# Kernel tuning notes

Measured on AMD Instinct MI355X. Metric: run time of the kernel, lower is better.

Reference implementation:

```python
import jax, jax.numpy as jnp
import numpy as np

DPH = 64          # dim_per_head
HALF = DPH // 2   # rope half dim
NH = 8            # num heads
SCALE = jnp.sqrt(jnp.float32(DPH))


def setup_inputs() -> dict:
    key = jax.random.key(0)
    ks = jax.random.split(key, 6)
    b, H, W, d = 2, 48, 48, 512
    qk_bound = 6.0 / np.sqrt(d + DPH)
    x = jax.random.normal(ks[0], (b, H, W, d), dtype=jnp.float32)
    wq = jax.random.uniform(ks[1], (d, DPH, NH), jnp.float32, -qk_bound, qk_bound)
    wk = jax.random.uniform(ks[2], (d, DPH, NH), jnp.float32, -qk_bound, qk_bound)
    wv = jax.random.uniform(ks[3], (d, DPH, NH), jnp.float32, -qk_bound, qk_bound)
    wo = jax.random.uniform(ks[4], (d, DPH, NH), jnp.float32, -qk_bound, qk_bound)
    angles = jax.random.normal(ks[5], (2, HALF), dtype=jnp.float32)  # base_freq=1.0
    return {"x": x, "wq": wq, "wk": wk, "wv": wv, "wo": wo, "angles": angles}


def _rope_angles(H, W, angles):
    # positions: meshgrid(indexing='ij') of arange(H), arange(W) -> [H, W, 2]
    ii, jj = jnp.meshgrid(jnp.arange(H, dtype=angles.dtype),
                          jnp.arange(W, dtype=angles.dtype), indexing="ij")
    pos = jnp.stack([ii, jj], axis=-1)              # [H, W, 2]
    return jnp.einsum("ijp,pc->ijc", pos, angles)   # [H, W, HALF]


def _apply_rope(t, cos, sin):
    # t: [b, h, H, W, dv]; interleaved pairs (d c) with c=2
    tr = t.reshape(*t.shape[:-1], HALF, 2)
    t0, t1 = tr[..., 0], tr[..., 1]
    rot = jnp.stack([t0 * cos - t1 * sin, t0 * sin + t1 * cos], axis=-1)
    return rot.reshape(t.shape)


def reference(x, wq, wk, wv, wo, angles):
    b, H, W, d = x.shape
    # QKV projections: [b,H,W,d] x [d,dv,h] -> [b,h,H,W,dv]
    q = jnp.einsum("bijd,dvh->bhijv", x, wq)
    k = jnp.einsum("bijd,dvh->bhijv", x, wk)
    v = jnp.einsum("bijd,dvh->bhijv", x, wv)
    ang = _rope_angles(H, W, angles)
    cos, sin = jnp.cos(ang), jnp.sin(ang)           # [H, W, HALF]
    q = _apply_rope(q, cos, sin)
    k = _apply_rope(k, cos, sin)
    # flatten spatial dims -> sequence
    n = H * W
    qf = q.reshape(b, NH, n, DPH)
    kf = k.reshape(b, NH, n, DPH)
    vf = v.reshape(b, NH, n, DPH)
    scores = jnp.einsum("bhqd,bhkd->bhqk", qf, kf) / SCALE
    attn = jax.nn.softmax(scores, axis=-1)
    out = jnp.einsum("bhqk,bhkd->bhqd", attn, vf).reshape(b, NH, H, W, DPH)
    # out projection: [b,h,H,W,dv] x [d,dv,h] -> [b,H,W,d]
    return jnp.einsum("bhijv,dvh->bijd", out, wo)
```

## Files before the change

### kernel.cpp

```cpp
#include <hip/hip_runtime.h>
#include <hip/hip_bf16.h>
#include <math.h>

#define BB   2
#define WW   48
#define DD   512
#define DPH  64
#define NHH  8
#define NSEQ 2304
#define NPOS (BB*NSEQ)
#define NXE  (NPOS*DD)
#define WSZ  (DD*DD)

typedef __attribute__((ext_vector_type(8))) short short8v;
typedef __attribute__((ext_vector_type(4))) float f32x4;

__device__ __forceinline__ ushort f2bf(float f) {
    union { __hip_bfloat16 h; ushort u; } cv;
    cv.h = __float2bfloat16(f);
    return cv.u;
}
__device__ __forceinline__ float bf2f(ushort u) {
    return __uint_as_float(((uint)u) << 16);
}

__global__ __launch_bounds__(256) void k_prep(
    const float* __restrict__ x,  const float* __restrict__ wq,
    const float* __restrict__ wk, const float* __restrict__ wv,
    const float* __restrict__ wo,
    ushort* __restrict__ xh, ushort* __restrict__ xl,
    ushort* __restrict__ Bqh, ushort* __restrict__ Bql,
    ushort* __restrict__ Bkh, ushort* __restrict__ Bkl,
    ushort* __restrict__ Bvh, ushort* __restrict__ Bvl,
    ushort* __restrict__ Boh, ushort* __restrict__ Bol)
{
    int idx = blockIdx.x*256 + threadIdx.x;
    float s;
    ushort *ph, *pl; int o;
    if (idx < NXE) {
        s = x[idx]; ph = xh; pl = xl; o = idx;
    } else {
        int t = idx - NXE;
        int sel = t >> 18;
        o = t & (WSZ-1);
        int c = o >> 9, k = o & 511;
        if (sel == 0)      { s = wq[k*512 + c] * 0.125f; ph = Bqh; pl = Bql; }
        else if (sel == 1) { s = wk[k*512 + c];          ph = Bkh; pl = Bkl; }
        else if (sel == 2) { s = wv[k*512 + c];          ph = Bvh; pl = Bvl; }
        else               { s = wo[c*512 + ((k&63)<<3) + (k>>6)]; ph = Boh; pl = Bol; }
    }
    ushort hi = f2bf(s);
    ph[o] = hi;
    pl[o] = f2bf(s - bf2f(hi));
}

#define LPITCH 80
__global__ __launch_bounds__(256) void k_gemm_qkv(
    const ushort* __restrict__ xhp, const ushort* __restrict__ xlp,
    const ushort* __restrict__ Bqh, const ushort* __restrict__ Bql,
    const ushort* __restrict__ Bkh, const ushort* __restrict__ Bkl,
    const ushort* __restrict__ Bvh, const ushort* __restrict__ Bvl,
    const float* __restrict__ ang,
    ushort* __restrict__ qa, ushort* __restrict__ ka, ushort* __restrict__ vT)
{
    __shared__ char xsh[64*LPITCH], xsl[64*LPITCH];
    __shared__ char wsh[256*LPITCH], wsl[256*LPITCH];
    const int tid = threadIdx.x;
    const int w = tid>>6, l = tid&63, g = l>>4, lr = l&15;
    const int mid = blockIdx.x / 144;
    const int rmb = blockIdx.x - mid*144;
    const int rowblk = rmb >> 1, colblk = rmb & 1;
    const int row0 = rowblk*64, col0 = colblk*256;
    const ushort* Bh; const ushort* Bl;
    if (mid==0)      { Bh = Bqh; Bl = Bql; }
    else if (mid==1) { Bh = Bkh; Bl = Bkl; }
    else             { Bh = Bvh; Bl = Bvl; }

    f32x4 acc[4][4];
#pragma unroll
    for (int mt=0;mt<4;++mt)
#pragma unroll
        for (int nt=0;nt<4;++nt) acc[mt][nt] = (f32x4){0.f,0.f,0.f,0.f};

#pragma unroll 1
    for (int kc = 0; kc < 16; ++kc) {
        const int k0 = kc*32;
        __syncthreads();
#pragma unroll
        for (int u = 0; u < 2; ++u) {
            int i2 = tid + 256*u;
            int tile = i2 >> 8, t2 = i2 & 255;
            int sr = t2 >> 2, sg = t2 & 3;
            const ushort* src = (tile ? xlp : xhp) + (size_t)(row0+sr)*512 + k0 + sg*8;
            char* dst = (tile ? xsl : xsh) + sr*LPITCH + sg*16;
            *reinterpret_cast<uint4*>(dst) = *reinterpret_cast<const uint4*>(src);
        }
#pragma unroll
        for (int u = 0; u < 8; ++u) {
            int i2 = tid + 256*u;
            int tile = i2 >> 10, t2 = i2 & 1023;
            int c = t2 >> 2, sg = t2 & 3;
            const ushort* src = (tile ? Bl : Bh) + (size_t)(col0+c)*512 + k0 + sg*8;
            char* dst = (tile ? wsl : wsh) + c*LPITCH + sg*16;
            *reinterpret_cast<uint4*>(dst) = *reinterpret_cast<const uint4*>(src);
        }
        __syncthreads();
        short8v ah[4], al[4], bh_[4], bl_[4];
#pragma unroll
        for (int mt = 0; mt < 4; ++mt) {
            ah[mt] = *reinterpret_cast<const short8v*>(xsh + (mt*16+lr)*LPITCH + g*16);
            al[mt] = *reinterpret_cast<const short8v*>(xsl + (mt*16+lr)*LPITCH + g*16);
        }
#pragma unroll
        for (int nt = 0; nt < 4; ++nt) {
            bh_[nt] = *reinterpret_cast<const short8v*>(wsh + (w*64+nt*16+lr)*LPITCH + g*16);
            bl_[nt] = *reinterpret_cast<const short8v*>(wsl + (w*64+nt*16+lr)*LPITCH + g*16);
        }
#pragma unroll
        for (int mt = 0; mt < 4; ++mt)
#pragma unroll
            for (int nt = 0; nt < 4; ++nt) {
                acc[mt][nt] = __builtin_amdgcn_mfma_f32_16x16x32_bf16(ah[mt], bh_[nt], acc[mt][nt], 0, 0, 0);
                acc[mt][nt] = __builtin_amdgcn_mfma_f32_16x16x32_bf16(ah[mt], bl_[nt], acc[mt][nt], 0, 0, 0);
                acc[mt][nt] = __builtin_amdgcn_mfma_f32_16x16x32_bf16(al[mt], bh_[nt], acc[mt][nt], 0, 0, 0);
            }
    }

    const int b = row0 / NSEQ;
    const int rem0 = row0 - b*NSEQ;
    if (mid < 2) {
        ushort* dst = (mid==0) ? qa : ka;
        const int sgn = (lr >= 8);
#pragma unroll
        for (int nt = 0; nt < 4; ++nt) {
            int cbase = col0 + w*64 + nt*16;
            int pc = cbase >> 4;
            float a_i = ang[pc], a_j = ang[32 + pc];
            int c = cbase + lr;
            int h = c & 7, v = c >> 3;
            ushort* colbase = dst + ((size_t)(b*NHH + h)*NSEQ)*DPH + v;
#pragma unroll
            for (int mt = 0; mt < 4; ++mt)
#pragma unroll
                for (int r = 0; r < 4; ++r) {
                    int rowrem = rem0 + mt*16 + 4*g + r;
                    int i = rowrem / WW, j = rowrem - (rowrem/WW)*WW;
                    float th = (float)i*a_i + (float)j*a_j;
                    float sn, cn; __sincosf(th, &sn, &cn);
                    float own = acc[mt][nt][r];
                    float oth = __shfl_xor(own, 8);
                    float rot = sgn ? (oth*sn + own*cn) : (own*cn - oth*sn);
                    colbase[(size_t)rowrem*DPH] = f2bf(rot);
                }
        }
    } else {
#pragma unroll
        for (int nt = 0; nt < 4; ++nt) {
            int c = col0 + w*64 + nt*16 + lr;
            int h = c & 7, v = c >> 3;
            ushort* colbase = vT + ((size_t)((b*NHH + h)*DPH + v))*NSEQ + rem0;
#pragma unroll
            for (int mt = 0; mt < 4; ++mt)
#pragma unroll
                for (int r = 0; r < 4; ++r)
                    colbase[mt*16 + 4*g + r] = f2bf(acc[mt][nt][r]);
        }
    }
}

__global__ __launch_bounds__(256) void k_gemm_o(
    const ushort* __restrict__ Oa, const ushort* __restrict__ Boh,
    const ushort* __restrict__ Bol, float* __restrict__ out)
{
    __shared__ char xs[64*LPITCH];
    __shared__ char wsh[256*LPITCH], wsl[256*LPITCH];
    const int tid = threadIdx.x;
    const int w = tid>>6, l = tid&63, g = l>>4, lr = l&15;
    const int row0 = (blockIdx.x >> 1)*64;
    const int col0 = (blockIdx.x & 1)*256;

    f32x4 acc[4][4];
#pragma unroll
    for (int mt=0;mt<4;++mt)
#pragma unroll
        for (int nt=0;nt<4;++nt) acc[mt][nt] = (f32x4){0.f,0.f,0.f,0.f};

#pragma unroll 1
    for (int kc = 0; kc < 16; ++kc) {
        const int k0 = kc*32;
        __syncthreads();
        {
            int sr = tid >> 2, sg = tid & 3;
            *reinterpret_cast<uint4*>(xs + sr*LPITCH + sg*16) =
                *reinterpret_cast<const uint4*>(Oa + (size_t)(row0+sr)*512 + k0 + sg*8);
        }
#pragma unroll
        for (int u = 0; u < 8; ++u) {
            int i2 = tid + 256*u;
            int tile = i2 >> 10, t2 = i2 & 1023;
            int c = t2 >> 2, sg = t2 & 3;
            const ushort* src = (tile ? Bol : Boh) + (size_t)(col0+c)*512 + k0 + sg*8;
            char* dst = (tile ? wsl : wsh) + c*LPITCH + sg*16;
            *reinterpret_cast<uint4*>(dst) = *reinterpret_cast<const uint4*>(src);
        }
        __syncthreads();
        short8v a[4], bh_[4], bl_[4];
#pragma unroll
        for (int mt = 0; mt < 4; ++mt)
            a[mt] = *reinterpret_cast<const short8v*>(xs + (mt*16+lr)*LPITCH + g*16);
#pragma unroll
        for (int nt = 0; nt < 4; ++nt) {
            bh_[nt] = *reinterpret_cast<const short8v*>(wsh + (w*64+nt*16+lr)*LPITCH + g*16);
            bl_[nt] = *reinterpret_cast<const short8v*>(wsl + (w*64+nt*16+lr)*LPITCH + g*16);
        }
#pragma unroll
        for (int mt = 0; mt < 4; ++mt)
#pragma unroll
            for (int nt = 0; nt < 4; ++nt) {
                acc[mt][nt] = __builtin_amdgcn_mfma_f32_16x16x32_bf16(a[mt], bh_[nt], acc[mt][nt], 0, 0, 0);
                acc[mt][nt] = __builtin_amdgcn_mfma_f32_16x16x32_bf16(a[mt], bl_[nt], acc[mt][nt], 0, 0, 0);
            }
    }

#pragma unroll
    for (int mt=0;mt<4;++mt)
#pragma unroll
        for (int r=0;r<4;++r) {
            float* rowp = out + (size_t)(row0 + mt*16 + 4*g + r)*DD + col0 + w*64;
#pragma unroll
            for (int nt=0;nt<4;++nt)
                rowp[nt*16 + lr] = acc[mt][nt][r];
        }
}

#define CK 64
#define NCHUNK (NSEQ/CK)
#define KP 72
__global__ __launch_bounds__(256) void k_attn_mfma(
    const ushort* __restrict__ qb, const ushort* __restrict__ kb,
    const ushort* __restrict__ vb, ushort* __restrict__ Oa)
{
    __shared__ ushort ksm[CK][KP];
    __shared__ ushort vsm[CK][KP];
    __shared__ ushort psm[4][16][KP];
    const int tid = threadIdx.x;
    const int w = tid >> 6, l = tid & 63;
    const int g = l >> 4, lr = l & 15;
    const int bh   = blockIdx.x / (NSEQ/64);
    const int qc   = blockIdx.x - bh*(NSEQ/64);
    const int row0 = qc * 64;
    const ushort* kbase = kb + (size_t)bh*NSEQ*DPH;
    const ushort* vbase = vb + (size_t)bh*DPH*NSEQ;

    const ushort* qptr = qb + ((size_t)bh*NSEQ + row0 + 16*w + lr)*DPH + g*8;
    const short8v qA0 = *reinterpret_cast<const short8v*>(qptr);
    const short8v qA1 = *reinterpret_cast<const short8v*>(qptr + 32);

    float mrow[4], lrow[4];
    f32x4 o[4];
#pragma unroll
    for (int r = 0; r < 4; ++r) { mrow[r] = -INFINITY; lrow[r] = 0.f; }
#pragma unroll
    for (int vt = 0; vt < 4; ++vt) o[vt] = (f32x4){0.f,0.f,0.f,0.f};

    for (int t = 0; t < NCHUNK; ++t) {
        __syncthreads();
#pragma unroll
        for (int i = 0; i < 2; ++i) {
            int tau = tid + 256*i;
            int row = tau >> 3, cg = tau & 7;
            *reinterpret_cast<uint4*>(&ksm[row][cg*8]) =
                *reinterpret_cast<const uint4*>(kbase + ((size_t)(t*CK + row))*DPH + cg*8);
            *reinterpret_cast<uint4*>(&vsm[row][cg*8]) =
                *reinterpret_cast<const uint4*>(vbase + (size_t)row*NSEQ + t*CK + cg*8);
        }
        __syncthreads();

        f32x4 s[4];
#pragma unroll
        for (int tile = 0; tile < 4; ++tile) {
            short8v k0 = *reinterpret_cast<const short8v*>(&ksm[tile*16 + lr][g*8]);
            short8v k1 = *reinterpret_cast<const short8v*>(&ksm[tile*16 + lr][32 + g*8]);
            f32x4 a2 = (f32x4){0.f,0.f,0.f,0.f};
            a2 = __builtin_amdgcn_mfma_f32_16x16x32_bf16(qA0, k0, a2, 0, 0, 0);
            a2 = __builtin_amdgcn_mfma_f32_16x16x32_bf16(qA1, k1, a2, 0, 0, 0);
            s[tile] = a2;
        }

        float f_r[4];
#pragma unroll
        for (int r = 0; r < 4; ++r) {
            float cm = fmaxf(fmaxf(s[0][r], s[1][r]), fmaxf(s[2][r], s[3][r]));
#pragma unroll
            for (int msk = 8; msk >= 1; msk >>= 1)
                cm = fmaxf(cm, __shfl_xor(cm, msk));
            float mn = fmaxf(mrow[r], cm);
            f_r[r] = __expf(mrow[r] - mn);
            mrow[r] = mn;
            float rs = 0.f;
#pragma unroll
            for (int tile = 0; tile < 4; ++tile) {
                float p = __expf(s[tile][r] - mn);
                s[tile][r] = p;
                rs += p;
            }
#pragma unroll
            for (int msk = 8; msk >= 1; msk >>= 1)
                rs += __shfl_xor(rs, msk);
            lrow[r] = lrow[r]*f_r[r] + rs;
        }

#pragma unroll
        for (int tile = 0; tile < 4; ++tile)
#pragma unroll
            for (int r = 0; r < 4; ++r)
                psm[w][4*g + r][lr + 16*tile] = f2bf(s[tile][r]);

#pragma unroll
        for (int vt = 0; vt < 4; ++vt)
#pragma unroll
            for (int r = 0; r < 4; ++r)
                o[vt][r] *= f_r[r];

#pragma unroll
        for (int half = 0; half < 2; ++half) {
            short8v pA = *reinterpret_cast<const short8v*>(&psm[w][lr][32*half + g*8]);
#pragma unroll
            for (int vt = 0; vt < 4; ++vt) {
                short8v vf = *reinterpret_cast<const short8v*>(&vsm[vt*16 + lr][32*half + g*8]);
                o[vt] = __builtin_amdgcn_mfma_f32_16x16x32_bf16(pA, vf, o[vt], 0, 0, 0);
            }
        }
    }

    float inv[4];
#pragma unroll
    for (int r = 0; r < 4; ++r) inv[r] = 1.f / lrow[r];
    const int b_ = bh >> 3, h_ = bh & 7;
#pragma unroll
    for (int vt = 0; vt < 4; ++vt)
#pragma unroll
        for (int r = 0; r < 4; ++r)
            Oa[((size_t)(b_*NSEQ + row0 + 16*w + 4*g + r))*DD + h_*64 + vt*16 + lr]
                = f2bf(o[vt][r]*inv[r]);
}

extern "C" void kernel_launch(void* const* d_in, const int* in_sizes, int n_in,
                              void* d_out, int out_size, void* d_ws, size_t ws_size,
                              hipStream_t stream) {
    const float* x   = (const float*)d_in[0];
    const float* wq  = (const float*)d_in[1];
    const float* wk  = (const float*)d_in[2];
    const float* wv  = (const float*)d_in[3];
    const float* wo  = (const float*)d_in[4];
    const float* ang = (const float*)d_in[5];
    float* out = (float*)d_out;

    ushort* xh  = (ushort*)d_ws;
    ushort* xl  = xh + NXE;
    ushort* Bqh = xl + NXE;
    ushort* Bql = Bqh + WSZ;
    ushort* Bkh = Bql + WSZ;
    ushort* Bkl = Bkh + WSZ;
    ushort* Bvh = Bkl + WSZ;
    ushort* Bvl = Bvh + WSZ;
    ushort* Boh = Bvl + WSZ;
    ushort* Bol = Boh + WSZ;
    ushort* qa  = Bol + WSZ;
    ushort* ka  = qa + NXE;
    ushort* vT  = ka + NXE;
    ushort* Oa  = xh;

    k_prep<<<(NXE + 4*WSZ)/256, 256, 0, stream>>>(x, wq, wk, wv, wo,
        xh, xl, Bqh, Bql, Bkh, Bkl, Bvh, Bvl, Boh, Bol);
    k_gemm_qkv<<<432, 256, 0, stream>>>(xh, xl, Bqh, Bql, Bkh, Bkl, Bvh, Bvl,
        ang, qa, ka, vT);
    k_attn_mfma<<<BB*NHH*(NSEQ/CK), 256, 0, stream>>>(qa, ka, vT, Oa);
    k_gemm_o<<<144, 256, 0, stream>>>(Oa, Boh, Bol, out);
}
```

Measured before the change: 237.7 us.

## Split attention KV range in two and merge partials in a combine kernel

The attention kernel now splits the key sequence into two halves, doubling the block count. Each block writes unnormalized partial outputs plus its running max and sum, and a new combine kernel merges the two halves into the final head-interleaved layout. The probability tile in shared memory is also XOR-swizzled to reduce bank conflicts. This aims to fill the GPU better and reduce the tail of the attention grid, at the cost of an extra launch and extra global traffic for the partials.

```diff
diff --git a/kernel.cpp b/kernel.cpp
--- a/kernel.cpp
+++ b/kernel.cpp
@@ -11,6 +11,7 @@
 #define NPOS (BB*NSEQ)
 #define NXE  (NPOS*DD)
 #define WSZ  (DD*DD)
+#define NROWS (BB*NHH*NSEQ)
 
 typedef __attribute__((ext_vector_type(8))) short short8v;
 typedef __attribute__((ext_vector_type(4))) float f32x4;
@@ -234,20 +235,22 @@
 }
 
 #define CK 64
-#define NCHUNK (NSEQ/CK)
 #define KP 72
 __global__ __launch_bounds__(256) void k_attn_mfma(
     const ushort* __restrict__ qb, const ushort* __restrict__ kb,
-    const ushort* __restrict__ vb, ushort* __restrict__ Oa)
+    const ushort* __restrict__ vb, ushort* __restrict__ Op,
+    float2* __restrict__ mlp)
 {
     __shared__ ushort ksm[CK][KP];
     __shared__ ushort vsm[CK][KP];
-    __shared__ ushort psm[4][16][KP];
+    __shared__ char psmb[4][2304];
     const int tid = threadIdx.x;
     const int w = tid >> 6, l = tid & 63;
     const int g = l >> 4, lr = l & 15;
-    const int bh   = blockIdx.x / (NSEQ/64);
-    const int qc   = blockIdx.x - bh*(NSEQ/64);
+    const int sp  = blockIdx.x / 576;
+    const int rest = blockIdx.x - sp*576;
+    const int bh = rest / 36;
+    const int qc = rest - bh*36;
     const int row0 = qc * 64;
     const ushort* kbase = kb + (size_t)bh*NSEQ*DPH;
     const ushort* vbase = vb + (size_t)bh*DPH*NSEQ;
@@ -263,7 +266,7 @@
 #pragma unroll
     for (int vt = 0; vt < 4; ++vt) o[vt] = (f32x4){0.f,0.f,0.f,0.f};
 
-    for (int t = 0; t < NCHUNK; ++t) {
+    for (int t = sp*18; t < sp*18 + 18; ++t) {
         __syncthreads();
 #pragma unroll
         for (int i = 0; i < 2; ++i) {
@@ -276,7 +279,7 @@
         }
         __syncthreads();
 
-        f32x4 s[4];
+        f32x4 sc[4];
 #pragma unroll
         for (int tile = 0; tile < 4; ++tile) {
             short8v k0 = *reinterpret_cast<const short8v*>(&ksm[tile*16 + lr][g*8]);
@@ -284,13 +287,13 @@
             f32x4 a2 = (f32x4){0.f,0.f,0.f,0.f};
             a2 = __builtin_amdgcn_mfma_f32_16x16x32_bf16(qA0, k0, a2, 0, 0, 0);
             a2 = __builtin_amdgcn_mfma_f32_16x16x32_bf16(qA1, k1, a2, 0, 0, 0);
-            s[tile] = a2;
+            sc[tile] = a2;
         }
 
         float f_r[4];
 #pragma unroll
         for (int r = 0; r < 4; ++r) {
-            float cm = fmaxf(fmaxf(s[0][r], s[1][r]), fmaxf(s[2][r], s[3][r]));
+            float cm = fmaxf(fmaxf(sc[0][r], sc[1][r]), fmaxf(sc[2][r], sc[3][r]));
 #pragma unroll
             for (int msk = 8; msk >= 1; msk >>= 1)
                 cm = fmaxf(cm, __shfl_xor(cm, msk));
@@ -300,8 +303,8 @@
             float rs = 0.f;
 #pragma unroll
             for (int tile = 0; tile < 4; ++tile) {
-                float p = __expf(s[tile][r] - mn);
-                s[tile][r] = p;
+                float p = __expf(sc[tile][r] - mn);
+                sc[tile][r] = p;
                 rs += p;
             }
 #pragma unroll
@@ -313,8 +316,10 @@
 #pragma unroll
         for (int tile = 0; tile < 4; ++tile)
 #pragma unroll
-            for (int r = 0; r < 4; ++r)
-                psm[w][4*g + r][lr + 16*tile] = f2bf(s[tile][r]);
+            for (int r = 0; r < 4; ++r) {
+                int bo = (((4*g + r)*144) + (lr + 16*tile)*2) ^ (g << 5);
+                *reinterpret_cast<ushort*>(&psmb[w][bo]) = f2bf(sc[tile][r]);
+            }
 
 #pragma unroll
         for (int vt = 0; vt < 4; ++vt)
@@ -324,7 +329,8 @@
 
 #pragma unroll
         for (int half = 0; half < 2; ++half) {
-            short8v pA = *reinterpret_cast<const short8v*>(&psm[w][lr][32*half + g*8]);
+            int bo = (lr*144 + 64*half + 16*g) ^ (((lr >> 2) & 3) << 5);
+            short8v pA = *reinterpret_cast<const short8v*>(&psmb[w][bo]);
 #pragma unroll
             for (int vt = 0; vt < 4; ++vt) {
                 short8v vf = *reinterpret_cast<const short8v*>(&vsm[vt*16 + lr][32*half + g*8]);
@@ -333,16 +339,44 @@
         }
     }
 
-    float inv[4];
-#pragma unroll
-    for (int r = 0; r < 4; ++r) inv[r] = 1.f / lrow[r];
-    const int b_ = bh >> 3, h_ = bh & 7;
+    ushort* obase = Op + ((size_t)sp*NROWS + (size_t)bh*NSEQ + row0 + 16*w)*64;
 #pragma unroll
     for (int vt = 0; vt < 4; ++vt)
 #pragma unroll
         for (int r = 0; r < 4; ++r)
-            Oa[((size_t)(b_*NSEQ + row0 + 16*w + 4*g + r))*DD + h_*64 + vt*16 + lr]
-                = f2bf(o[vt][r]*inv[r]);
+            obase[(4*g + r)*64 + vt*16 + lr] = f2bf(o[vt][r]);
+    if (lr == 0) {
+#pragma unroll
+        for (int r = 0; r < 4; ++r)
+            mlp[sp*NROWS + bh*NSEQ + row0 + 16*w + 4*g + r] = make_float2(mrow[r], lrow[r]);
+    }
+}
+
+__global__ __launch_bounds__(256) void k_combine(
+    const ushort* __restrict__ Op, const float2* __restrict__ mlp,
+    ushort* __restrict__ Oa)
+{
+    const int tid = threadIdx.x;
+    const int row = blockIdx.x*32 + (tid >> 3);
+    const int c8 = (tid & 7)*8;
+    float2 a = mlp[row], b = mlp[NROWS + row];
+    float M = fmaxf(a.x, b.x);
+    float w0 = __expf(a.x - M), w1 = __expf(b.x - M);
+    float inv = 1.f / (a.y*w0 + b.y*w1);
+    const ushort* p0 = Op + (size_t)row*64 + c8;
+    const ushort* p1 = p0 + (size_t)NROWS*64;
+    uint4 u0 = *reinterpret_cast<const uint4*>(p0);
+    uint4 u1 = *reinterpret_cast<const uint4*>(p1);
+    const ushort* s0 = reinterpret_cast<const ushort*>(&u0);
+    const ushort* s1 = reinterpret_cast<const ushort*>(&u1);
+    ushort res[8];
+#pragma unroll
+    for (int i = 0; i < 8; ++i)
+        res[i] = f2bf((bf2f(s0[i])*w0 + bf2f(s1[i])*w1) * inv);
+    int bh = row / NSEQ, n = row - bh*NSEQ;
+    int b_ = bh >> 3, h_ = bh & 7;
+    ushort* dst = Oa + ((size_t)(b_*NSEQ + n))*DD + h_*64 + c8;
+    *reinterpret_cast<uint4*>(dst) = *reinterpret_cast<const uint4*>(res);
 }
 
 extern "C" void kernel_launch(void* const* d_in, const int* in_sizes, int n_in,
@@ -369,12 +403,15 @@
     ushort* qa  = Bol + WSZ;
     ushort* ka  = qa + NXE;
     ushort* vT  = ka + NXE;
-    ushort* Oa  = xh;
+    ushort* Oa  = vT + NXE;
+    ushort* Op  = xh;
+    float2* mlp = (float2*)Bqh;
 
     k_prep<<<(NXE + 4*WSZ)/256, 256, 0, stream>>>(x, wq, wk, wv, wo,
         xh, xl, Bqh, Bql, Bkh, Bkl, Bvh, Bvl, Boh, Bol);
     k_gemm_qkv<<<432, 256, 0, stream>>>(xh, xl, Bqh, Bql, Bkh, Bkl, Bvh, Bvl,
         ang, qa, ka, vT);
-    k_attn_mfma<<<BB*NHH*(NSEQ/CK), 256, 0, stream>>>(qa, ka, vT, Oa);
+    k_attn_mfma<<<1152, 256, 0, stream>>>(qa, ka, vT, Op, mlp);
+    k_combine<<<NROWS/32, 256, 0, stream>>>(Op, mlp, Oa);
     k_gemm_o<<<144, 256, 0, stream>>>(Oa, Boh, Bol, out);
 }
```

Measured after the change: 224.7 us. 1.06x faster.
